# Performance work log

Hardware: AMD Instinct MI355X
Metric: run time of the kernel (lower is better)

## Reference

```python
import jax, jax.numpy as jnp
import numpy as np

B, S, HID = 2, 2048, 2048
H, KV, D = 16, 4, 128
G = H // KV  # kv groups
THETA = 10000.0


def setup_inputs() -> dict:
    key = jax.random.key(0)
    ks = jax.random.split(key, 6)
    x = jax.random.normal(ks[0], (B, S, HID), dtype=jnp.float32)
    wq = jax.random.normal(ks[1], (HID, H * D), dtype=jnp.float32) * 0.02
    wk = jax.random.normal(ks[2], (HID, KV * D), dtype=jnp.float32) * 0.02
    wv = jax.random.normal(ks[3], (HID, KV * D), dtype=jnp.float32) * 0.02
    wo = jax.random.normal(ks[4], (H * D, HID), dtype=jnp.float32) * 0.02
    # RoPE freqs: complex exp(i * pos * theta^{-2j/D}) -> cos/sin of shape [S, D//2]
    inv_freq = 1.0 / (THETA ** (jnp.arange(0, D, 2, dtype=jnp.float32) / D))
    ang = jnp.arange(S, dtype=jnp.float32)[:, None] * inv_freq[None, :]
    return {"x": x, "freqs_cos": jnp.cos(ang), "freqs_sin": jnp.sin(ang),
            "wq": wq, "wk": wk, "wv": wv, "wo": wo}


def _apply_rope(t, cos, sin):
    # t: [B, h, S, D]; cos/sin: [S, D//2]; complex multiply on interleaved pairs
    tr = t.reshape(*t.shape[:-1], -1, 2)
    x1, x2 = tr[..., 0], tr[..., 1]
    c = cos[None, None, :, :]
    s = sin[None, None, :, :]
    out = jnp.stack([x1 * c - x2 * s, x1 * s + x2 * c], axis=-1)
    return out.reshape(t.shape)


def reference(x, freqs_cos, freqs_sin, wq, wk, wv, wo):
    b, s, _ = x.shape
    q = (x @ wq).reshape(b, s, H, D).transpose(0, 2, 1, 3)   # [B,H,S,D]
    k = (x @ wk).reshape(b, s, KV, D).transpose(0, 2, 1, 3)  # [B,KV,S,D]
    v = (x @ wv).reshape(b, s, KV, D).transpose(0, 2, 1, 3)
    q = _apply_rope(q, freqs_cos, freqs_sin)
    k = _apply_rope(k, freqs_cos, freqs_sin)
    # GQA: group Q heads per KV head instead of expanding K/V
    qg = q.reshape(b, KV, G, s, D)
    scale = 1.0 / jnp.sqrt(jnp.asarray(D, dtype=x.dtype))
    scores = jnp.einsum('bkgqd,bksd->bkgqs', qg, k) * scale  # [B,KV,G,S,S]
    causal = jnp.tril(jnp.ones((s, s), dtype=bool))
    scores = jnp.where(causal[None, None, None], scores, jnp.finfo(scores.dtype).min)
    attn = jax.nn.softmax(scores, axis=-1)
    out = jnp.einsum('bkgqs,bksd->bkgqd', attn, v)           # [B,KV,G,S,D]
    out = out.reshape(b, H, s, D).transpose(0, 2, 1, 3).reshape(b, s, H * D)
    return (out @ wo, k, v)
```

## Files before the change

### kernel.cpp

```cpp
#include <hip/hip_runtime.h>
#include <stdint.h>

#define BB 2
#define SS 2048
#define HIDD 2048
#define HH 16
#define KVH 4
#define DD 128
#define KDIM 2048

typedef short bf16x4 __attribute__((ext_vector_type(4)));
typedef short bf16x8 __attribute__((ext_vector_type(8)));
typedef float f32x4 __attribute__((ext_vector_type(4)));
typedef float f32x16 __attribute__((ext_vector_type(16)));

__device__ __forceinline__ unsigned short f2b(float f) {
  union { float f; unsigned u; } v; v.f = f;
  unsigned r = v.u + 0x7FFFu + ((v.u >> 16) & 1u);
  return (unsigned short)(r >> 16);
}

__device__ __forceinline__ unsigned cvtpk_bf16(float a, float b) {
  unsigned r;
  asm("v_cvt_pk_bf16_f32 %0, %1, %2" : "=v"(r) : "v"(a), "v"(b));
  return r;
}

__device__ __forceinline__ void gload16(const unsigned short* g, unsigned short* l) {
  __builtin_amdgcn_global_load_lds(
      (const __attribute__((address_space(1))) unsigned int*)(g),
      (__attribute__((address_space(3))) unsigned int*)(l), 16, 0, 0);
}

__device__ __forceinline__ bf16x8 ldT(const char* lds, int byteoff) {
  union { bf16x8 v; int4 q; } u;
  u.q = *reinterpret_cast<const int4*>(lds + byteoff);
  return u.v;
}


__global__ __launch_bounds__(256) void k_convert(const float* __restrict__ in,
                                                 unsigned short* __restrict__ out, int n4) {
  int i = blockIdx.x * 256 + threadIdx.x;
  int stride = gridDim.x * 256;
  for (; i < n4; i += stride) {
    float4 v = reinterpret_cast<const float4*>(in)[i];
    ushort4 o;
    o.x = f2b(v.x); o.y = f2b(v.y); o.z = f2b(v.z); o.w = f2b(v.w);
    int ci = i & 511;
    int t = ci & 7;
    int ci2 = (ci & ~7) | ((t & 3) << 1) | (t >> 2);
    reinterpret_cast<ushort4*>(out)[(i & ~511) | ci2] = o;
  }
}

__global__ __launch_bounds__(256) void k_transpose(const float* __restrict__ in,
                                                   unsigned short* __restrict__ out,
                                                   int K, int N) {
  __shared__ float tile[32][33];
  int n0 = blockIdx.x * 32, k0 = blockIdx.y * 32;
  int tx = threadIdx.x, ty = threadIdx.y;
#pragma unroll
  for (int j = 0; j < 32; j += 8)
    tile[ty + j][tx] = in[(size_t)(k0 + ty + j) * N + n0 + tx];
  __syncthreads();
  int kp = ((tx >> 2) & 3) * 8 + (tx & 3) + ((tx >> 4) << 2);
#pragma unroll
  for (int j = 0; j < 32; j += 8)
    out[(size_t)(n0 + ty + j) * K + k0 + kp] = f2b(tile[tx][ty + j]);
}

template <int EPI>
__global__ __launch_bounds__(256) void k_gemm(
    const unsigned short* __restrict__ A, const unsigned short* __restrict__ Bt,
    float* __restrict__ outF, unsigned short* __restrict__ qws,
    unsigned short* __restrict__ kws, unsigned short* __restrict__ vTws,
    float* __restrict__ koutF, float* __restrict__ voutF,
    const float* __restrict__ cosT, const float* __restrict__ sinT) {
  __shared__ __align__(16) unsigned short lA[2][128 * 32];
  __shared__ __align__(16) unsigned short lB[2][128 * 32];
  const int rowbase = blockIdx.x * 128;
  const int colbase = blockIdx.y * 128;
  const int t = threadIdx.x;
  const int wid = t >> 6, lane = t & 63;
  const int g = lane >> 4, c = lane & 15;
  const int wrow = (wid >> 1) * 64, wcol = (wid & 1) * 64;

  const int rloc = lane >> 2, sslot = lane & 3;

  f32x4 acc[4][4] = {};

  const int NT = KDIM / 32;

  auto STAGE = [&](int buf, int kt) {
    const int kbase = kt * 32;
#pragma unroll
    for (int j = 0; j < 2; ++j) {
      int r = wid * 32 + j * 16 + rloc;
      int gch = sslot ^ ((r >> 1) & 3);
      gload16(A + (size_t)(rowbase + r) * KDIM + kbase + gch * 8,
              &lA[buf][(wid * 32 + j * 16) * 32]);
      gload16(Bt + (size_t)(colbase + r) * KDIM + kbase + gch * 8,
              &lB[buf][(wid * 32 + j * 16) * 32]);
    }
  };

  STAGE(0, 0);
  __syncthreads();

  for (int kt = 0; kt < NT; ++kt) {
    const int cur = kt & 1;
    if (kt + 1 < NT) STAGE(cur ^ 1, kt + 1);

    const unsigned short* la = lA[cur];
    const unsigned short* lb = lB[cur];
    bf16x8 af[4], bfm[4];
#pragma unroll
    for (int m = 0; m < 4; ++m) {
      int r = wrow + m * 16 + c;
      int slot = g ^ ((r >> 1) & 3);
      af[m] = *reinterpret_cast<const bf16x8*>(la + r * 32 + slot * 8);
    }
#pragma unroll
    for (int n = 0; n < 4; ++n) {
      int r = wcol + n * 16 + c;
      int slot = g ^ ((r >> 1) & 3);
      bfm[n] = *reinterpret_cast<const bf16x8*>(lb + r * 32 + slot * 8);
    }
#pragma unroll
    for (int m = 0; m < 4; ++m)
#pragma unroll
      for (int n = 0; n < 4; ++n)
        acc[m][n] = __builtin_amdgcn_mfma_f32_16x16x32_bf16(af[m], bfm[n], acc[m][n], 0, 0, 0);
    __syncthreads();
  }

  if (EPI == 0) {
#pragma unroll
    for (int m = 0; m < 4; ++m)
#pragma unroll
      for (int n = 0; n < 4; ++n)
#pragma unroll
        for (int i = 0; i < 4; ++i) {
          int R = rowbase + wrow + m * 16 + g * 4 + i;
          int Cc = colbase + wcol + n * 16 + c;
          outF[(size_t)R * 2048 + Cc] = acc[m][n][i];
        }
  } else {
#pragma unroll
    for (int m = 0; m < 4; ++m) {
#pragma unroll
      for (int n = 0; n < 4; ++n) {
#pragma unroll
        for (int i = 0; i < 4; ++i) {
          float val = acc[m][n][i];
          float partner = __shfl_xor(val, 1, 64);
          int R = rowbase + wrow + m * 16 + g * 4 + i;
          int Cc = colbase + wcol + n * 16 + c;
          int b = R >> 11, s = R & 2047;
          int d = Cc & 127;
          int j = d >> 1;
          float cs = cosT[s * 64 + j], sn = sinT[s * 64 + j];
          float ro = ((d & 1) == 0) ? (val * cs - partner * sn)
                                    : (partner * sn + val * cs);
          if (Cc < 2048) {
            int h = Cc >> 7;
            qws[((size_t)(b * HH + h) * SS + s) * DD + d] = f2b(ro);
          } else if (Cc < 2560) {
            int kvh = (Cc - 2048) >> 7;
            size_t idx = ((size_t)(b * KVH + kvh) * SS + s) * DD + d;
            koutF[idx] = ro;
            kws[idx] = f2b(ro);
          } else {
            int kvh = (Cc - 2560) >> 7;
            size_t idx = ((size_t)(b * KVH + kvh) * SS + s) * DD + d;
            voutF[idx] = val;
            vTws[((size_t)(b * KVH + kvh) * DD + d) * SS + s] = f2b(val);
          }
        }
      }
    }
  }
}

__global__ __launch_bounds__(256, 2) void k_attn(const unsigned short* __restrict__ qws,
                                                 const unsigned short* __restrict__ kws,
                                                 const unsigned short* __restrict__ vT,
                                                 unsigned short* __restrict__ aows) {
  __shared__ __align__(16) char lds[2][32768];
  const int tid = threadIdx.x;
  const int lane = tid & 63;
  const int w = tid >> 6;
  const int lq = lane & 31;
  const int hi = lane >> 5;

  const int bid = blockIdx.x;
  const int chunk = (bid < 256) ? (15 - (bid >> 5)) : ((bid - 256) >> 5);
  const int head = bid & 31;
  const int b = head >> 4, h = head & 15;
  const int kv = h >> 2;
  const int q0 = chunk * 128;
  const int q0w = q0 + w * 32;
  const int qg = q0w + lq;
  const int NT = chunk * 2 + 2;
  const float cl2 = 0.12751743f;

  const unsigned short* qp = qws + ((size_t)(b * HH + h) * SS + qg) * DD;
  bf16x8 qf[8];
#pragma unroll
  for (int ks = 0; ks < 8; ++ks) {
    union { bf16x8 v8; bf16x4 v4[2]; } u;
    const unsigned short* p = qp + ks * 16 + hi * 4;
    u.v4[0] = *reinterpret_cast<const bf16x4*>(p);
    u.v4[1] = *reinterpret_cast<const bf16x4*>(p + 8);
    qf[ks] = u.v8;
  }

  const unsigned short* kbase = kws + (size_t)(b * KVH + kv) * SS * DD;
  const unsigned short* vbase = vT + (size_t)(b * KVH + kv) * DD * SS;

  const int krow = tid >> 2, kslB = tid & 3;
  const int vrow = tid >> 1, vslB = tid & 1;
  int2 kreg[8], vreg[8];

  auto ISSUE = [&](int t) {
    const int kb = t * 64;
#pragma unroll
    for (int ss = 0; ss < 4; ++ss) {
      int sl = kslB + ss * 4, ks = sl >> 1, h2 = sl & 1;
      const unsigned short* src = kbase + (size_t)(kb + krow) * DD + ks * 16 + h2 * 4;
      kreg[2 * ss]     = *reinterpret_cast<const int2*>(src);
      kreg[2 * ss + 1] = *reinterpret_cast<const int2*>(src + 8);
    }
#pragma unroll
    for (int ss = 0; ss < 4; ++ss) {
      int sl = vslB + ss * 2, kk = sl >> 1, h2 = sl & 1;
      const unsigned short* src = vbase + (size_t)vrow * SS + kb + kk * 16 + h2 * 4;
      vreg[2 * ss]     = *reinterpret_cast<const int2*>(src);
      vreg[2 * ss + 1] = *reinterpret_cast<const int2*>(src + 8);
    }
  };
  auto WRITE = [&](int buf) {
    char* lK = lds[buf];
    char* lV = lds[buf] + 16384;
#pragma unroll
    for (int ss = 0; ss < 4; ++ss) {
      int sl = kslB + ss * 4, ks = sl >> 1, h2 = sl & 1;
      int off = (krow * 256 + ks * 32 + h2 * 16) ^ ((krow & 15) << 4);
      int4 wv; wv.x = kreg[2*ss].x; wv.y = kreg[2*ss].y; wv.z = kreg[2*ss+1].x; wv.w = kreg[2*ss+1].y;
      *reinterpret_cast<int4*>(lK + off) = wv;
    }
#pragma unroll
    for (int ss = 0; ss < 4; ++ss) {
      int sl = vslB + ss * 2, kk = sl >> 1, h2 = sl & 1;
      int off = (vrow * 128 + kk * 32 + h2 * 16) ^ ((vrow & 15) << 4);
      int4 wv; wv.x = vreg[2*ss].x; wv.y = vreg[2*ss].y; wv.z = vreg[2*ss+1].x; wv.w = vreg[2*ss+1].y;
      *reinterpret_cast<int4*>(lV + off) = wv;
    }
  };

  f32x16 o[4] = {};
  float mrow = -1e30f, lrow = 0.f;

  ISSUE(0);
  WRITE(0);
  __syncthreads();

  for (int t = 0; t < NT; ++t) {
    const bool more = (t + 1 < NT);
    if (more) ISSUE(t + 1);

    if (t * 64 <= q0w + 31) {
      const char* lK = lds[t & 1];
      const char* lV = lds[t & 1] + 16384;
      const int swz = ((lq & 15) << 4);

      f32x16 s[2];
      __builtin_amdgcn_s_setprio(1);
#pragma unroll
      for (int mf = 0; mf < 2; ++mf) {
        f32x16 acc = {};
#pragma unroll
        for (int ks = 0; ks < 8; ++ks) {
          int off = ((mf * 32 + lq) * 256 + ks * 32 + hi * 16) ^ swz;
          acc = __builtin_amdgcn_mfma_f32_32x32x16_bf16(ldT(lK, off), qf[ks], acc, 0, 0, 0);
        }
        s[mf] = acc;
      }
      __builtin_amdgcn_s_setprio(0);

      const bool needMask = (t * 64 + 63) > q0w;
      const int kq = t * 64 + 4 * hi - qg;
      float p[32];
      float rowmax = -1e30f;
#pragma unroll
      for (int mf = 0; mf < 2; ++mf)
#pragma unroll
        for (int r = 0; r < 16; ++r) {
          float v = s[mf][r] * cl2;
          if (needMask) {
            int kl = mf * 32 + (r & 3) + 8 * (r >> 2);
            if (kq + kl > 0) v = -1e30f;
          }
          p[mf * 16 + r] = v;
          rowmax = fmaxf(rowmax, v);
        }
      rowmax = fmaxf(rowmax, __shfl_xor(rowmax, 32, 64));

      if (__any(rowmax > mrow + 8.f)) {
        float mnew = fmaxf(mrow, rowmax);
        float fac = exp2f(mrow - mnew);
        mrow = mnew;
        lrow *= fac;
#pragma unroll
        for (int d0 = 0; d0 < 4; ++d0)
#pragma unroll
          for (int r = 0; r < 16; ++r) o[d0][r] *= fac;
      }

      float rsum = 0.f;
#pragma unroll
      for (int e = 0; e < 32; ++e) { p[e] = exp2f(p[e] - mrow); rsum += p[e]; }
      rsum += __shfl_xor(rsum, 32, 64);
      lrow += rsum;

      bf16x8 pf[4];
#pragma unroll
      for (int s4 = 0; s4 < 4; ++s4) {
        union { bf16x8 v; unsigned u[4]; } pu;
        int base = (s4 >> 1) * 16 + (s4 & 1) * 8;
#pragma unroll
        for (int j = 0; j < 4; ++j)
          pu.u[j] = cvtpk_bf16(p[base + 2 * j], p[base + 2 * j + 1]);
        pf[s4] = pu.v;
      }

      __builtin_amdgcn_s_setprio(1);
#pragma unroll
      for (int d0 = 0; d0 < 4; ++d0)
#pragma unroll
        for (int kk = 0; kk < 4; ++kk) {
          int off = ((d0 * 32 + lq) * 128 + kk * 32 + hi * 16) ^ swz;
          o[d0] = __builtin_amdgcn_mfma_f32_32x32x16_bf16(ldT(lV, off), pf[kk], o[d0], 0, 0, 0);
        }
      __builtin_amdgcn_s_setprio(0);
    }

    if (more) {
      WRITE((t + 1) & 1);
      __syncthreads();
    }
  }

  float linv = 1.f / lrow;
  unsigned short* op = aows + ((size_t)(b * SS + qg)) * 2048 + h * 128;
#pragma unroll
  for (int d0 = 0; d0 < 4; ++d0)
#pragma unroll
    for (int rq = 0; rq < 4; ++rq) {
      unsigned w0 = cvtpk_bf16(o[d0][rq * 4 + 0] * linv, o[d0][rq * 4 + 1] * linv);
      unsigned w1 = cvtpk_bf16(o[d0][rq * 4 + 2] * linv, o[d0][rq * 4 + 3] * linv);
      int2 st2; st2.x = (int)w0; st2.y = (int)w1;
      int pos = 8 * ((2 * rq + hi) & 3) + 4 * (rq >> 1);
      *reinterpret_cast<int2*>(op + d0 * 32 + pos) = st2;
    }
}

extern "C" void kernel_launch(void* const* d_in, const int* in_sizes, int n_in,
                              void* d_out, int out_size, void* d_ws, size_t ws_size,
                              hipStream_t stream) {
  (void)in_sizes; (void)n_in; (void)out_size; (void)ws_size;
  const float* x  = (const float*)d_in[0];
  const float* fc = (const float*)d_in[1];
  const float* fs = (const float*)d_in[2];
  const float* wq = (const float*)d_in[3];
  const float* wk = (const float*)d_in[4];
  const float* wv = (const float*)d_in[5];
  const float* wo = (const float*)d_in[6];
  float* out = (float*)d_out;
  float* koutF = out + (size_t)BB * SS * HIDD;
  float* voutF = koutF + (size_t)BB * KVH * SS * DD;

  unsigned short* wcatT = (unsigned short*)d_ws;
  unsigned short* woT   = wcatT + (size_t)3072 * 2048;
  unsigned short* xbf   = woT + (size_t)2048 * 2048;
  unsigned short* qws   = xbf + (size_t)4096 * 2048;
  unsigned short* kws   = qws + (size_t)BB * HH * SS * DD;
  unsigned short* vTws  = kws + (size_t)BB * KVH * SS * DD;
  unsigned short* aows  = vTws + (size_t)BB * KVH * DD * SS;

  k_convert<<<2048, 256, 0, stream>>>(x, xbf, (int)((size_t)4096 * 2048 / 4));
  dim3 tb(32, 8);
  k_transpose<<<dim3(64, 64), tb, 0, stream>>>(wq, wcatT, 2048, 2048);
  k_transpose<<<dim3(16, 64), tb, 0, stream>>>(wk, wcatT + (size_t)2048 * 2048, 2048, 512);
  k_transpose<<<dim3(16, 64), tb, 0, stream>>>(wv, wcatT + (size_t)2560 * 2048, 2048, 512);
  k_transpose<<<dim3(64, 64), tb, 0, stream>>>(wo, woT, 2048, 2048);

  k_gemm<1><<<dim3(32, 24), 256, 0, stream>>>(xbf, wcatT, nullptr, qws, kws, vTws,
                                              koutF, voutF, fc, fs);
  k_attn<<<512, 256, 0, stream>>>(qws, kws, vTws, aows);
  k_gemm<0><<<dim3(32, 16), 256, 0, stream>>>(aows, woT, out, nullptr, nullptr, nullptr,
                                              nullptr, nullptr, nullptr, nullptr);
}
```

Measured before the change: 254.6 us.

## Skip masked half-tiles, single-buffer LDS, and remap block-to-head ordering

The attention kernel now skips the second 32-key half of a 64-key tile when it lies entirely above the causal diagonal for a wave, avoiding wasted MFMAs, exp and conversions. LDS drops from double to single buffering, which adds an extra barrier per iteration but halves shared memory and lifts the launch-bounds occupancy hint. Block indexing is simplified to a single descending-chunk order, and heads are remapped so blocks sharing a KV head are spread apart. The extra sync may serialize loads and compute more than before.

```diff
diff --git a/kernel.cpp b/kernel.cpp
--- a/kernel.cpp
+++ b/kernel.cpp
@@ -183,11 +183,11 @@
   }
 }
 
-__global__ __launch_bounds__(256, 2) void k_attn(const unsigned short* __restrict__ qws,
-                                                 const unsigned short* __restrict__ kws,
-                                                 const unsigned short* __restrict__ vT,
-                                                 unsigned short* __restrict__ aows) {
-  __shared__ __align__(16) char lds[2][32768];
+__global__ __launch_bounds__(256) void k_attn(const unsigned short* __restrict__ qws,
+                                              const unsigned short* __restrict__ kws,
+                                              const unsigned short* __restrict__ vT,
+                                              unsigned short* __restrict__ aows) {
+  __shared__ __align__(16) char lds[32768];
   const int tid = threadIdx.x;
   const int lane = tid & 63;
   const int w = tid >> 6;
@@ -195,12 +195,12 @@
   const int hi = lane >> 5;
 
   const int bid = blockIdx.x;
-  const int chunk = (bid < 256) ? (15 - (bid >> 5)) : ((bid - 256) >> 5);
-  const int head = bid & 31;
+  const int chunk = 15 - (bid >> 5);
+  const int y = bid & 31;
+  const int head = 4 * (y & 7) + ((y >> 3) & 3);
   const int b = head >> 4, h = head & 15;
   const int kv = h >> 2;
-  const int q0 = chunk * 128;
-  const int q0w = q0 + w * 32;
+  const int q0w = chunk * 128 + w * 32;
   const int qg = q0w + lq;
   const int NT = chunk * 2 + 2;
   const float cl2 = 0.12751743f;
@@ -240,9 +240,9 @@
       vreg[2 * ss + 1] = *reinterpret_cast<const int2*>(src + 8);
     }
   };
-  auto WRITE = [&](int buf) {
-    char* lK = lds[buf];
-    char* lV = lds[buf] + 16384;
+  auto WRITE = [&]() {
+    char* lK = lds;
+    char* lV = lds + 16384;
 #pragma unroll
     for (int ss = 0; ss < 4; ++ss) {
       int sl = kslB + ss * 4, ks = sl >> 1, h2 = sl & 1;
@@ -263,7 +263,7 @@
   float mrow = -1e30f, lrow = 0.f;
 
   ISSUE(0);
-  WRITE(0);
+  WRITE();
   __syncthreads();
 
   for (int t = 0; t < NT; ++t) {
@@ -271,40 +271,54 @@
     if (more) ISSUE(t + 1);
 
     if (t * 64 <= q0w + 31) {
-      const char* lK = lds[t & 1];
-      const char* lV = lds[t & 1] + 16384;
+      const char* lK = lds;
+      const char* lV = lds + 16384;
       const int swz = ((lq & 15) << 4);
-
-      f32x16 s[2];
+      const bool full2 = (t * 64 + 32 <= q0w + 31);
+
+      f32x16 s0 = {}, s1 = {};
       __builtin_amdgcn_s_setprio(1);
 #pragma unroll
-      for (int mf = 0; mf < 2; ++mf) {
-        f32x16 acc = {};
+      for (int ks = 0; ks < 8; ++ks) {
+        int off = (lq * 256 + ks * 32 + hi * 16) ^ swz;
+        s0 = __builtin_amdgcn_mfma_f32_32x32x16_bf16(ldT(lK, off), qf[ks], s0, 0, 0, 0);
+      }
+      if (full2) {
 #pragma unroll
         for (int ks = 0; ks < 8; ++ks) {
-          int off = ((mf * 32 + lq) * 256 + ks * 32 + hi * 16) ^ swz;
-          acc = __builtin_amdgcn_mfma_f32_32x32x16_bf16(ldT(lK, off), qf[ks], acc, 0, 0, 0);
-        }
-        s[mf] = acc;
+          int off = ((32 + lq) * 256 + ks * 32 + hi * 16) ^ swz;
+          s1 = __builtin_amdgcn_mfma_f32_32x32x16_bf16(ldT(lK, off), qf[ks], s1, 0, 0, 0);
+        }
       }
       __builtin_amdgcn_s_setprio(0);
 
-      const bool needMask = (t * 64 + 63) > q0w;
       const int kq = t * 64 + 4 * hi - qg;
       float p[32];
       float rowmax = -1e30f;
-#pragma unroll
-      for (int mf = 0; mf < 2; ++mf)
+      const bool m0 = (t * 64 + 31) > q0w;
+#pragma unroll
+      for (int r = 0; r < 16; ++r) {
+        float v = s0[r] * cl2;
+        if (m0) {
+          int kl = (r & 3) + 8 * (r >> 2);
+          if (kq + kl > 0) v = -1e30f;
+        }
+        p[r] = v;
+        rowmax = fmaxf(rowmax, v);
+      }
+      if (full2) {
+        const bool m1 = (t * 64 + 63) > q0w;
 #pragma unroll
         for (int r = 0; r < 16; ++r) {
-          float v = s[mf][r] * cl2;
-          if (needMask) {
-            int kl = mf * 32 + (r & 3) + 8 * (r >> 2);
+          float v = s1[r] * cl2;
+          if (m1) {
+            int kl = 32 + (r & 3) + 8 * (r >> 2);
             if (kq + kl > 0) v = -1e30f;
           }
-          p[mf * 16 + r] = v;
+          p[16 + r] = v;
           rowmax = fmaxf(rowmax, v);
         }
+      }
       rowmax = fmaxf(rowmax, __shfl_xor(rowmax, 32, 64));
 
       if (__any(rowmax > mrow + 8.f)) {
@@ -320,34 +334,59 @@
 
       float rsum = 0.f;
 #pragma unroll
-      for (int e = 0; e < 32; ++e) { p[e] = exp2f(p[e] - mrow); rsum += p[e]; }
+      for (int e = 0; e < 16; ++e) { p[e] = exp2f(p[e] - mrow); rsum += p[e]; }
+      if (full2) {
+#pragma unroll
+        for (int e = 16; e < 32; ++e) { p[e] = exp2f(p[e] - mrow); rsum += p[e]; }
+      }
       rsum += __shfl_xor(rsum, 32, 64);
       lrow += rsum;
 
       bf16x8 pf[4];
 #pragma unroll
-      for (int s4 = 0; s4 < 4; ++s4) {
+      for (int s4 = 0; s4 < 2; ++s4) {
         union { bf16x8 v; unsigned u[4]; } pu;
-        int base = (s4 >> 1) * 16 + (s4 & 1) * 8;
+        int base = s4 * 8;
 #pragma unroll
         for (int j = 0; j < 4; ++j)
           pu.u[j] = cvtpk_bf16(p[base + 2 * j], p[base + 2 * j + 1]);
         pf[s4] = pu.v;
       }
+      if (full2) {
+#pragma unroll
+        for (int s4 = 2; s4 < 4; ++s4) {
+          union { bf16x8 v; unsigned u[4]; } pu;
+          int base = 16 + (s4 - 2) * 8;
+#pragma unroll
+          for (int j = 0; j < 4; ++j)
+            pu.u[j] = cvtpk_bf16(p[base + 2 * j], p[base + 2 * j + 1]);
+          pf[s4] = pu.v;
+        }
+      }
 
       __builtin_amdgcn_s_setprio(1);
 #pragma unroll
       for (int d0 = 0; d0 < 4; ++d0)
 #pragma unroll
-        for (int kk = 0; kk < 4; ++kk) {
+        for (int kk = 0; kk < 2; ++kk) {
           int off = ((d0 * 32 + lq) * 128 + kk * 32 + hi * 16) ^ swz;
           o[d0] = __builtin_amdgcn_mfma_f32_32x32x16_bf16(ldT(lV, off), pf[kk], o[d0], 0, 0, 0);
         }
+      if (full2) {
+#pragma unroll
+        for (int d0 = 0; d0 < 4; ++d0)
+#pragma unroll
+          for (int kk = 2; kk < 4; ++kk) {
+            int off = ((d0 * 32 + lq) * 128 + kk * 32 + hi * 16) ^ swz;
+            o[d0] = __builtin_amdgcn_mfma_f32_32x32x16_bf16(ldT(lV, off), pf[kk], o[d0], 0, 0, 0);
+          }
+      }
       __builtin_amdgcn_s_setprio(0);
     }
 
+    __syncthreads();
     if (more) {
-      WRITE((t + 1) & 1);
+      WRITE();
       __syncthreads();
     }
   }
```

New measurement: 274.6 us. 1.08x slower.
